# Optimization experiments

Measured on AMD Instinct MI355X. Metric: run time of the kernel, lower is better.

Reference implementation:

```python
import jax, jax.numpy as jnp
import numpy as np

N, E, P, D = 100000, 800000, 100000, 128

def setup_inputs() -> dict:
    key = jax.random.key(0)
    ks = jax.random.split(key, 24)
    def w(k, i, o):
        return jax.random.normal(k, (i, o), jnp.float32) * (1.0 / np.sqrt(i))
    inp = {
        'x': jax.random.normal(ks[0], (N, D), jnp.float32),
        'src': jax.random.randint(ks[1], (E,), 0, N, jnp.int32),
        'dst': jax.random.randint(ks[2], (E,), 0, N, jnp.int32),
        'pos_src': jax.random.randint(ks[3], (P,), 0, N, jnp.int32),
        'pos_dst': jax.random.randint(ks[4], (P,), 0, N, jnp.int32),
        'neg_src': jax.random.randint(ks[5], (P,), 0, N, jnp.int32),
        'neg_dst': jax.random.randint(ks[6], (P,), 0, N, jnp.int32),
        # SAGEConv params: fc_self, fc_neigh (+bias) per layer
        'Ws0': w(ks[7], D, D), 'Wn0': w(ks[8], D, D), 'b0': jnp.zeros((D,), jnp.float32),
        'Ws1': w(ks[9], D, D), 'Wn1': w(ks[10], D, D), 'b1': jnp.zeros((D,), jnp.float32),
        'Ws2': w(ks[11], D, D), 'Wn2': w(ks[12], D, D), 'b2': jnp.zeros((D,), jnp.float32),
        # predictor MLP: D->D->D->2
        'Wp0': w(ks[13], D, D), 'bp0': jnp.zeros((D,), jnp.float32),
        'Wp1': w(ks[14], D, D), 'bp1': jnp.zeros((D,), jnp.float32),
        'Wp2': w(ks[15], D, 2), 'bp2': jnp.zeros((2,), jnp.float32),
    }
    return inp

def _sage_layer(h, src, dst, n, Ws, Wn, b, act):
    # mean aggregation over in-neighbors (gather -> segment_sum -> divide)
    msum = jax.ops.segment_sum(h[src], dst, num_segments=n)      # [N, D]
    deg = jax.ops.segment_sum(jnp.ones_like(dst, jnp.float32), dst, num_segments=n)
    h_neigh = msum / jnp.maximum(deg, 1.0)[:, None]
    out = h @ Ws + h_neigh @ Wn + b
    return jax.nn.relu(out) if act else out

def _predict(hs, hd, Wp0, bp0, Wp1, bp1, Wp2, bp2):
    z = hs * hd
    z = jax.nn.relu(z @ Wp0 + bp0)
    z = jax.nn.relu(z @ Wp1 + bp1)
    return jax.nn.softmax(z @ Wp2 + bp2, axis=1)[:, 1]

def reference(x, src, dst, pos_src, pos_dst, neg_src, neg_dst,
              Ws0, Wn0, b0, Ws1, Wn1, b1, Ws2, Wn2, b2,
              Wp0, bp0, Wp1, bp1, Wp2, bp2):
    n = x.shape[0]
    h = _sage_layer(x, src, dst, n, Ws0, Wn0, b0, True)
    h = _sage_layer(h, src, dst, n, Ws1, Wn1, b1, True)
    h = _sage_layer(h, src, dst, n, Ws2, Wn2, b2, False)
    pos = _predict(h[pos_src], h[pos_dst], Wp0, bp0, Wp1, bp1, Wp2, bp2)
    neg = _predict(h[neg_src], h[neg_dst], Wp0, bp0, Wp1, bp1, Wp2, bp2)
    return (pos, neg)
```

## Files before the change

kernel.cpp:

```cpp
#include <hip/hip_runtime.h>
#include <cstdint>
#include <cstddef>
#include <cmath>

#define D 128

typedef short bf16x8 __attribute__((ext_vector_type(8)));
typedef float f32x4 __attribute__((ext_vector_type(4)));

__device__ __forceinline__ ushort f2b(float f) {
  uint x = __float_as_uint(f);
  uint r = ((x >> 16) & 1u) + 0x7fffu;
  return (ushort)((x + r) >> 16);
}
__device__ __forceinline__ float b2f(ushort u) {
  return __uint_as_float(((uint)u) << 16);
}

__device__ __forceinline__ void gl2lds16(const void* g, void* l) {
  __builtin_amdgcn_global_load_lds(
      (__attribute__((address_space(1))) void*)const_cast<void*>(g),
      (__attribute__((address_space(3))) void*)l, 16, 0, 0);
}

#define DB 1024
__global__ __launch_bounds__(256) void k_degree_conv(
    const int* __restrict__ dst, int E, int* __restrict__ deg,
    const float* __restrict__ in, ushort* __restrict__ outx, int n8, int cb,
    const float* __restrict__ Ws0, const float* __restrict__ Wn0,
    const float* __restrict__ Ws1, const float* __restrict__ Wn1,
    const float* __restrict__ Ws2, const float* __restrict__ Wn2,
    const float* __restrict__ Wp0, const float* __restrict__ Wp1,
    ushort* __restrict__ BpL0, ushort* __restrict__ BpL1, ushort* __restrict__ BpL2,
    ushort* __restrict__ BpP0, ushort* __restrict__ BpP1) {
  int b = blockIdx.x;
  if (b < DB) {
    for (int e = b * 256 + (int)threadIdx.x; e < E; e += DB * 256)
      atomicAdd(&deg[dst[e]], 1);
    return;
  }
  int b2 = b - DB;
  if (b2 < cb) {
    int i = b2 * 256 + threadIdx.x;
    if (i >= n8) return;
    float4 a = ((const float4*)in)[i * 2];
    float4 c = ((const float4*)in)[i * 2 + 1];
    ushort4 o0 = {f2b(a.x), f2b(a.y), f2b(a.z), f2b(a.w)};
    ushort4 o1 = {f2b(c.x), f2b(c.y), f2b(c.z), f2b(c.w)};
    ((ushort4*)outx)[i * 2] = o0;
    ((ushort4*)outx)[i * 2 + 1] = o1;
    return;
  }
  int o = (b2 - cb) * 256 + threadIdx.x;
  const float *W0, *W1; ushort* outp; int rel;
  if (o < 32768)       { W0 = Ws0; W1 = Wn0; outp = BpL0; rel = o; }
  else if (o < 65536)  { W0 = Ws1; W1 = Wn1; outp = BpL1; rel = o - 32768; }
  else if (o < 98304)  { W0 = Ws2; W1 = Wn2; outp = BpL2; rel = o - 65536; }
  else if (o < 114688) { W0 = Wp0; W1 = Wp0; outp = BpP0; rel = o - 98304; }
  else                 { W0 = Wp1; W1 = Wp1; outp = BpP1; rel = o - 114688; }
  int j = rel & 7, lane = (rel >> 3) & 63, t = (rel >> 9) & 7, ks = rel >> 12;
  int k = ks * 32 + ((lane >> 4) * 8) + j;
  int n = t * 16 + (lane & 15);
  const float* W = (k < 128) ? W0 : W1;
  int kk = (k < 128) ? k : k - 128;
  outp[rel] = f2b(W[(size_t)kk * D + n]);
}

__global__ __launch_bounds__(256) void k_fill_p(const int* __restrict__ src,
    const int* __restrict__ dst, int E, int* __restrict__ cursor,
    int* __restrict__ csrc, float scale, int CE) {
  int part = blockIdx.x & 7, chunk = blockIdx.x >> 3;
  long base = (long)chunk * CE;
  for (int i = threadIdx.x; i < CE; i += 256) {
    long e = base + i;
    if (e < E) {
      int d = dst[e];
      int p = (int)((float)d * scale); if (p > 7) p = 7;
      if (p == part) {
        int s = src[e];
        int pos = atomicAdd(&cursor[d], 1);
        csrc[pos] = s;
      }
    }
  }
}

#define SCAN_T 256
#define SCAN_E 4
#define SCAN_CHUNK (SCAN_T * SCAN_E)

__global__ void k_scan_partial(const int* __restrict__ deg, int n, int* __restrict__ part) {
  __shared__ int s[SCAN_T];
  int base = blockIdx.x * SCAN_CHUNK;
  int sum = 0;
  for (int i = 0; i < SCAN_E; ++i) {
    int idx = base + (int)threadIdx.x * SCAN_E + i;
    if (idx < n) sum += deg[idx];
  }
  s[threadIdx.x] = sum; __syncthreads();
  for (int ofs = SCAN_T / 2; ofs > 0; ofs >>= 1) {
    if ((int)threadIdx.x < ofs) s[threadIdx.x] += s[threadIdx.x + ofs];
    __syncthreads();
  }
  if (threadIdx.x == 0) part[blockIdx.x] = s[0];
}

__global__ void k_scan_final(const int* __restrict__ deg, int n, const int* __restrict__ part,
                             int nb, int* __restrict__ rowptr, int* __restrict__ cursor, int E) {
  __shared__ int s[SCAN_T];
  __shared__ int pbase;
  {
    int v = 0;
    for (int t = (int)threadIdx.x; t < (int)blockIdx.x; t += SCAN_T) v += part[t];
    s[threadIdx.x] = v; __syncthreads();
    for (int ofs = SCAN_T / 2; ofs > 0; ofs >>= 1) {
      if ((int)threadIdx.x < ofs) s[threadIdx.x] += s[threadIdx.x + ofs];
      __syncthreads();
    }
    if (threadIdx.x == 0) pbase = s[0];
    __syncthreads();
  }
  int base = blockIdx.x * SCAN_CHUNK;
  int v[SCAN_E]; int local = 0;
  for (int i = 0; i < SCAN_E; ++i) {
    int idx = base + (int)threadIdx.x * SCAN_E + i;
    v[i] = (idx < n) ? deg[idx] : 0;
    local += v[i];
  }
  s[threadIdx.x] = local; __syncthreads();
  for (int ofs = 1; ofs < SCAN_T; ofs <<= 1) {
    int t = ((int)threadIdx.x >= ofs) ? s[threadIdx.x - ofs] : 0;
    __syncthreads();
    s[threadIdx.x] += t;
    __syncthreads();
  }
  int run = pbase + s[threadIdx.x] - local;
  for (int i = 0; i < SCAN_E; ++i) {
    int idx = base + (int)threadIdx.x * SCAN_E + i;
    if (idx < n) { rowptr[idx] = run; cursor[idx] = run; }
    run += v[i];
  }
  if (blockIdx.x == 0 && threadIdx.x == 0) rowptr[n] = E;
}

#define SMS 136
__global__ __launch_bounds__(128, 4) void k_sage_fused(
    const ushort* __restrict__ A, const int* __restrict__ rowptr,
    const int* __restrict__ csrc, const ushort* __restrict__ Bp,
    const float* __restrict__ bias, ushort* __restrict__ out, int N, int do_relu) {
  __shared__ __align__(16) ushort smean[2][16][SMS];
  int tid = threadIdx.x, wave = tid >> 6, lane = tid & 63;
  int m = lane & 15, kg = lane >> 4;
  int g = kg, sub = m;
  int gb = g << 4;
  int row0 = (blockIdx.x * 2 + wave) * 16;
  uint hbo = (uint)(sub * 16);

  int node0 = row0 + g * 4;
  int rpv = 0;
  if (sub < 5) { int ix = node0 + sub; if (ix > N) ix = N; rpv = rowptr[ix]; }
  int beg[4], dgf[4], dd[4];
  #pragma unroll
  for (int j = 0; j < 4; ++j) {
    beg[j] = __shfl(rpv, gb + j);
    int endj = __shfl(rpv, gb + j + 1);
    dgf[j] = endj - beg[j];
    dd[j] = dgf[j] < 16 ? dgf[j] : 16;
  }
  int idxv[4];
  #pragma unroll
  for (int j = 0; j < 4; ++j) {
    int i = beg[j] + sub;
    idxv[j] = (sub < dgf[j]) ? csrc[i] : 0;
  }

  float f[4][8];
  #pragma unroll
  for (int j = 0; j < 4; ++j)
    #pragma unroll
    for (int q = 0; q < 8; ++q) f[j][q] = 0.f;

  int maxdd = dd[0];
  if (dd[1] > maxdd) maxdd = dd[1];
  if (dd[2] > maxdd) maxdd = dd[2];
  if (dd[3] > maxdd) maxdd = dd[3];

  uint off[4][4];
  #pragma unroll
  for (int j = 0; j < 4; ++j)
    #pragma unroll
    for (int k = 0; k < 4; ++k)
      off[j][k] = hbo + ((uint)__shfl(idxv[j], gb + k) << 8);

  #pragma unroll 1
  for (int e = 0; e < maxdd; e += 4) {
    bf16x8 r[4][4];
    #pragma unroll
    for (int j = 0; j < 4; ++j)
      #pragma unroll
      for (int k = 0; k < 4; ++k)
        r[j][k] = *(const bf16x8*)((const char*)A + off[j][k]);
    __builtin_amdgcn_sched_barrier(0);
    #pragma unroll
    for (int j = 0; j < 4; ++j)
      #pragma unroll
      for (int k = 0; k < 4; ++k) {
        int sl = e + 4 + k; sl = (sl > 15) ? 15 : sl;
        off[j][k] = hbo + ((uint)__shfl(idxv[j], gb + sl) << 8);
      }
    __builtin_amdgcn_sched_barrier(0);
    #pragma unroll
    for (int j = 0; j < 4; ++j) {
      #pragma unroll
      for (int k = 0; k < 4; ++k) {
        float w = (e + k < dd[j]) ? 1.0f : 0.0f;
        #pragma unroll
        for (int q = 0; q < 8; ++q) f[j][q] += w * b2f((ushort)r[j][k][q]);
      }
    }
  }
  #pragma unroll
  for (int j = 0; j < 4; ++j) {
    int endj = beg[j] + dgf[j];
    for (int i = beg[j] + 16; i < endj; ++i) {
      int s = csrc[i];
      bf16x8 v = *(const bf16x8*)((const char*)A + (hbo + ((uint)s << 8)));
      #pragma unroll
      for (int q = 0; q < 8; ++q) f[j][q] += b2f((ushort)v[q]);
    }
  }
  #pragma unroll
  for (int j = 0; j < 4; ++j) {
    float inv = (dgf[j] > 0) ? (1.0f / (float)dgf[j]) : 0.0f;
    bf16x8 o;
    #pragma unroll
    for (int q = 0; q < 8; ++q) o[q] = (short)f2b(f[j][q] * inv);
    *(bf16x8*)&smean[wave][g * 4 + j][sub * 8] = o;
  }
  asm volatile("s_waitcnt lgkmcnt(0)" ::: "memory");
  __builtin_amdgcn_sched_barrier(0);

  int ar = row0 + m; if (ar >= N) ar = N - 1;
  const ushort* a_self = A + (size_t)ar * D + kg * 8;
  f32x4 acc[8];
  #pragma unroll
  for (int t = 0; t < 8; ++t) acc[t] = f32x4{0.f, 0.f, 0.f, 0.f};
  #pragma unroll
  for (int ks = 0; ks < 8; ++ks) {
    bf16x8 af = (ks < 4) ? *(const bf16x8*)(a_self + ks * 32)
                         : *(const bf16x8*)&smean[wave][m][(ks - 4) * 32 + kg * 8];
    const ushort* bb = Bp + (size_t)ks * 4096 + lane * 8;
    #pragma unroll
    for (int t = 0; t < 8; ++t)
      acc[t] = __builtin_amdgcn_mfma_f32_16x16x32_bf16(af, *(const bf16x8*)(bb + t * 512), acc[t], 0, 0, 0);
  }
  #pragma unroll
  for (int t = 0; t < 8; ++t) {
    int c = t * 16 + m;
    float bv = bias[c];
    #pragma unroll
    for (int i = 0; i < 4; ++i) {
      int r = row0 + kg * 4 + i;
      float v = acc[t][i] + bv;
      if (do_relu) v = fmaxf(v, 0.f);
      if (r < N) out[(size_t)r * D + c] = f2b(v);
    }
  }
}

__global__ __launch_bounds__(256, 5) void k_predict_mfma(
    const ushort* __restrict__ h,
    const int* __restrict__ ps, const int* __restrict__ pd,
    const int* __restrict__ ns, const int* __restrict__ nd,
    const ushort* __restrict__ Bp0, const float* __restrict__ bp0,
    const ushort* __restrict__ Bp1, const float* __restrict__ bp1,
    const float* __restrict__ Wp2, const float* __restrict__ bp2,
    float* __restrict__ outp, int P, int pb) {
  __shared__ __align__(1024) ushort slab[4][4096];
  int bi = blockIdx.x;
  const int* sidx; const int* didx; float* op;
  if (bi >= pb) { sidx = ns; didx = nd; op = outp + P; bi -= pb; }
  else          { sidx = ps; didx = pd; op = outp; }
  int tid = threadIdx.x;
  int wave = tid >> 6, lane = tid & 63;
  int m = lane & 15, kg = lane >> 4;
  int pair0 = bi * 64 + wave * 16;
  int prow = pair0 + m; int pr = (prow < P) ? prow : P - 1;
  int si = sidx[pr], di = didx[pr];
  char* sl = (char*)&slab[wave][0];

  {
    int rsub = lane >> 4;
    #pragma unroll
    for (int q = 0; q < 4; ++q) {
      int rr = q * 4 + rsub;
      int ir = __shfl(si, rr);
      const char* g = (const char*)h + ((size_t)(uint)ir << 8)
                      + (uint)((((lane & 15) ^ (rr & 7)) << 4));
      gl2lds16(g, sl + (q << 10));
    }
    #pragma unroll
    for (int q = 0; q < 4; ++q) {
      int rr = q * 4 + rsub;
      int ir = __shfl(di, rr);
      const char* g = (const char*)h + ((size_t)(uint)ir << 8)
                      + (uint)((((lane & 15) ^ (rr & 7)) << 4));
      gl2lds16(g, sl + 4096 + (q << 10));
    }
  }
  __syncthreads();

  f32x4 acc[8];
  #pragma unroll
  for (int t = 0; t < 8; ++t) acc[t] = f32x4{0.f, 0.f, 0.f, 0.f};
  #pragma unroll
  for (int ks = 0; ks < 4; ++ks) {
    int slot = (ks * 4 + kg) ^ (m & 7);
    const char* rbase = sl + m * 256 + slot * 16;
    bf16x8 as8 = *(const bf16x8*)rbase;
    bf16x8 ad8 = *(const bf16x8*)(rbase + 4096);
    bf16x8 af;
    #pragma unroll
    for (int j = 0; j < 8; ++j) {
      float p = b2f((ushort)as8[j]) * b2f((ushort)ad8[j]);
      af[j] = (short)f2b(p);
    }
    const ushort* bb = Bp0 + (size_t)ks * 4096 + lane * 8;
    #pragma unroll
    for (int t = 0; t < 8; ++t)
      acc[t] = __builtin_amdgcn_mfma_f32_16x16x32_bf16(af, *(const bf16x8*)(bb + t * 512), acc[t], 0, 0, 0);
  }
  ushort* zp = (ushort*)sl;
  #pragma unroll
  for (int t = 0; t < 8; ++t) {
    int c = t * 16 + m;
    float bv = bp0[c];
    int ks2 = c >> 5, kg2 = (c >> 3) & 3, j2 = c & 7;
    #pragma unroll
    for (int i = 0; i < 4; ++i) {
      float v = fmaxf(acc[t][i] + bv, 0.f);
      int l2 = kg2 * 16 + kg * 4 + i;
      zp[(ks2 * 64 + l2) * 8 + j2] = f2b(v);
    }
  }
  asm volatile("s_waitcnt lgkmcnt(0)" ::: "memory");
  __builtin_amdgcn_sched_barrier(0);
  #pragma unroll
  for (int t = 0; t < 8; ++t) acc[t] = f32x4{0.f, 0.f, 0.f, 0.f};
  #pragma unroll
  for (int ks = 0; ks < 4; ++ks) {
    bf16x8 af = *(const bf16x8*)(zp + (ks * 64 + lane) * 8);
    const ushort* bb = Bp1 + (size_t)ks * 4096 + lane * 8;
    #pragma unroll
    for (int t = 0; t < 8; ++t)
      acc[t] = __builtin_amdgcn_mfma_f32_16x16x32_bf16(af, *(const bf16x8*)(bb + t * 512), acc[t], 0, 0, 0);
  }
  float p0[4] = {0.f, 0.f, 0.f, 0.f}, p1[4] = {0.f, 0.f, 0.f, 0.f};
  #pragma unroll
  for (int t = 0; t < 8; ++t) {
    int c = t * 16 + m;
    float bv = bp1[c];
    float wa = Wp2[(size_t)c * 2], wb = Wp2[(size_t)c * 2 + 1];
    #pragma unroll
    for (int i = 0; i < 4; ++i) {
      float z = fmaxf(acc[t][i] + bv, 0.f);
      p0[i] += z * wa;
      p1[i] += z * wb;
    }
  }
  #pragma unroll
  for (int msk = 1; msk <= 8; msk <<= 1) {
    #pragma unroll
    for (int i = 0; i < 4; ++i) {
      p0[i] += __shfl_xor(p0[i], msk);
      p1[i] += __shfl_xor(p1[i], msk);
    }
  }
  if (m == 0) {
    float c0 = bp2[0], c1 = bp2[1];
    #pragma unroll
    for (int i = 0; i < 4; ++i) {
      int r = pair0 + kg * 4 + i;
      if (r < P) {
        float l0 = p0[i] + c0, l1 = p1[i] + c1;
        op[r] = 1.0f / (1.0f + expf(l0 - l1));
      }
    }
  }
}

extern "C" void kernel_launch(void* const* d_in, const int* in_sizes, int n_in,
                              void* d_out, int out_size, void* d_ws, size_t ws_size,
                              hipStream_t stream) {
  const float* x       = (const float*)d_in[0];
  const int*   src     = (const int*)d_in[1];
  const int*   dst     = (const int*)d_in[2];
  const int*   pos_src = (const int*)d_in[3];
  const int*   pos_dst = (const int*)d_in[4];
  const int*   neg_src = (const int*)d_in[5];
  const int*   neg_dst = (const int*)d_in[6];
  const float* Ws0 = (const float*)d_in[7],  *Wn0 = (const float*)d_in[8],  *b0 = (const float*)d_in[9];
  const float* Ws1 = (const float*)d_in[10], *Wn1 = (const float*)d_in[11], *b1 = (const float*)d_in[12];
  const float* Ws2 = (const float*)d_in[13], *Wn2 = (const float*)d_in[14], *b2 = (const float*)d_in[15];
  const float* Wp0 = (const float*)d_in[16], *bp0 = (const float*)d_in[17];
  const float* Wp1 = (const float*)d_in[18], *bp1 = (const float*)d_in[19];
  const float* Wp2 = (const float*)d_in[20], *bp2 = (const float*)d_in[21];
  const int N = in_sizes[0] / D;
  const int E = in_sizes[1];
  const int P = in_sizes[3];
  float* outp = (float*)d_out;

  char* ws = (char*)d_ws;
  size_t off = 0;
  auto alloc = [&](size_t bytes) -> void* {
    void* p = ws + off;
    off += (bytes + 255) & ~(size_t)255;
    return p;
  };
  ushort* xb    = (ushort*)alloc((size_t)N * D * 2);
  ushort* h1    = (ushort*)alloc((size_t)N * D * 2);
  ushort* h2    = (ushort*)alloc((size_t)N * D * 2);
  ushort* BpL0  = (ushort*)alloc(256 * D * 2);
  ushort* BpL1  = (ushort*)alloc(256 * D * 2);
  ushort* BpL2  = (ushort*)alloc(256 * D * 2);
  ushort* BpP0  = (ushort*)alloc(128 * D * 2);
  ushort* BpP1  = (ushort*)alloc(128 * D * 2);
  int*    deg    = (int*)alloc((size_t)N * 4);
  int*    rowptr = (int*)alloc((size_t)(N + 1) * 4);
  int*    cursor = (int*)alloc((size_t)N * 4);
  int*    part   = (int*)alloc(4096);
  int*    csrc   = (int*)alloc((size_t)E * 4);
  (void)ws_size; (void)n_in; (void)out_size;

  const float pscale = 8.0f / (float)N;
  const int CB = 96;
  const int CE = (E + CB - 1) / CB;

  hipMemsetAsync(deg, 0, (size_t)N * 4, stream);
  int n8 = N * D / 8;
  int cb = (n8 + 255) / 256;
  k_degree_conv<<<DB + cb + 512, 256, 0, stream>>>(
      dst, E, deg,
      x, xb, n8, cb,
      Ws0, Wn0, Ws1, Wn1, Ws2, Wn2, Wp0, Wp1,
      BpL0, BpL1, BpL2, BpP0, BpP1);

  int nb = (N + SCAN_CHUNK - 1) / SCAN_CHUNK;
  k_scan_partial<<<nb, SCAN_T, 0, stream>>>(deg, N, part);
  k_scan_final<<<nb, SCAN_T, 0, stream>>>(deg, N, part, nb, rowptr, cursor, E);
  k_fill_p<<<8 * CB, 256, 0, stream>>>(src, dst, E, cursor, csrc, pscale, CE);

  int gemb = (N + 31) / 32;
  k_sage_fused<<<gemb, 128, 0, stream>>>(xb, rowptr, csrc, BpL0, b0, h1, N, 1);
  k_sage_fused<<<gemb, 128, 0, stream>>>(h1, rowptr, csrc, BpL1, b1, h2, N, 1);
  k_sage_fused<<<gemb, 128, 0, stream>>>(h2, rowptr, csrc, BpL2, b2, xb, N, 0);

  int pb = (P + 63) / 64;
  k_predict_mfma<<<2 * pb, 256, 0, stream>>>(xb, pos_src, pos_dst, neg_src, neg_dst,
                                             BpP0, bp0, BpP1, bp1, Wp2, bp2, outp, P, pb);
}
```

Measured before the change: 445.4 us.

## Replace CSR build with fixed-slot per-node adjacency and overflow spill list

Drops the degree-count, two-pass scan and separate fill kernels. Edges are instead written straight into 32 fixed slots per destination node, with a global spill list for any overflow, all inside the fused conversion kernel. This removes three launches and one full pass over the edge list. The cost is a padded adjacency array of N*32 ints with sparser gather reads, and a linear scan of the spill list for high-degree nodes. Edges are silently dropped if the spill list exceeds its cap.

```diff
diff --git a/kernel.cpp b/kernel.cpp
--- a/kernel.cpp
+++ b/kernel.cpp
@@ -4,6 +4,8 @@
 #include <cmath>
 
 #define D 128
+#define SLOTS 32
+#define SPILL_CAP 65536
 
 typedef short bf16x8 __attribute__((ext_vector_type(8)));
 typedef float f32x4 __attribute__((ext_vector_type(4)));
@@ -23,9 +25,11 @@
       (__attribute__((address_space(3))) void*)l, 16, 0, 0);
 }
 
-#define DB 1024
-__global__ __launch_bounds__(256) void k_degree_conv(
-    const int* __restrict__ dst, int E, int* __restrict__ deg,
+__global__ __launch_bounds__(256) void k_fill_conv(
+    const int* __restrict__ src, const int* __restrict__ dst, int E,
+    int* __restrict__ cnt, int* __restrict__ csrc,
+    int* __restrict__ spillc, int* __restrict__ spill_d, int* __restrict__ spill_s,
+    float scale, int CE,
     const float* __restrict__ in, ushort* __restrict__ outx, int n8, int cb,
     const float* __restrict__ Ws0, const float* __restrict__ Wn0,
     const float* __restrict__ Ws1, const float* __restrict__ Wn1,
@@ -34,12 +38,29 @@
     ushort* __restrict__ BpL0, ushort* __restrict__ BpL1, ushort* __restrict__ BpL2,
     ushort* __restrict__ BpP0, ushort* __restrict__ BpP1) {
   int b = blockIdx.x;
-  if (b < DB) {
-    for (int e = b * 256 + (int)threadIdx.x; e < E; e += DB * 256)
-      atomicAdd(&deg[dst[e]], 1);
+  if (b < 768) {
+    int part = b & 7, chunk = b >> 3;
+    long base = (long)chunk * CE;
+    for (int i = threadIdx.x; i < CE; i += 256) {
+      long e = base + i;
+      if (e < E) {
+        int d = dst[e];
+        int p = (int)((float)d * scale); if (p > 7) p = 7;
+        if (p == part) {
+          int s = src[e];
+          int pos = atomicAdd(&cnt[d], 1);
+          if (pos < SLOTS) {
+            csrc[((size_t)d << 5) + pos] = s;
+          } else {
+            int si = atomicAdd(spillc, 1);
+            if (si < SPILL_CAP) { spill_d[si] = d; spill_s[si] = s; }
+          }
+        }
+      }
+    }
     return;
   }
-  int b2 = b - DB;
+  int b2 = b - 768;
   if (b2 < cb) {
     int i = b2 * 256 + threadIdx.x;
     if (i >= n8) return;
@@ -66,87 +87,12 @@
   outp[rel] = f2b(W[(size_t)kk * D + n]);
 }
 
-__global__ __launch_bounds__(256) void k_fill_p(const int* __restrict__ src,
-    const int* __restrict__ dst, int E, int* __restrict__ cursor,
-    int* __restrict__ csrc, float scale, int CE) {
-  int part = blockIdx.x & 7, chunk = blockIdx.x >> 3;
-  long base = (long)chunk * CE;
-  for (int i = threadIdx.x; i < CE; i += 256) {
-    long e = base + i;
-    if (e < E) {
-      int d = dst[e];
-      int p = (int)((float)d * scale); if (p > 7) p = 7;
-      if (p == part) {
-        int s = src[e];
-        int pos = atomicAdd(&cursor[d], 1);
-        csrc[pos] = s;
-      }
-    }
-  }
-}
-
-#define SCAN_T 256
-#define SCAN_E 4
-#define SCAN_CHUNK (SCAN_T * SCAN_E)
-
-__global__ void k_scan_partial(const int* __restrict__ deg, int n, int* __restrict__ part) {
-  __shared__ int s[SCAN_T];
-  int base = blockIdx.x * SCAN_CHUNK;
-  int sum = 0;
-  for (int i = 0; i < SCAN_E; ++i) {
-    int idx = base + (int)threadIdx.x * SCAN_E + i;
-    if (idx < n) sum += deg[idx];
-  }
-  s[threadIdx.x] = sum; __syncthreads();
-  for (int ofs = SCAN_T / 2; ofs > 0; ofs >>= 1) {
-    if ((int)threadIdx.x < ofs) s[threadIdx.x] += s[threadIdx.x + ofs];
-    __syncthreads();
-  }
-  if (threadIdx.x == 0) part[blockIdx.x] = s[0];
-}
-
-__global__ void k_scan_final(const int* __restrict__ deg, int n, const int* __restrict__ part,
-                             int nb, int* __restrict__ rowptr, int* __restrict__ cursor, int E) {
-  __shared__ int s[SCAN_T];
-  __shared__ int pbase;
-  {
-    int v = 0;
-    for (int t = (int)threadIdx.x; t < (int)blockIdx.x; t += SCAN_T) v += part[t];
-    s[threadIdx.x] = v; __syncthreads();
-    for (int ofs = SCAN_T / 2; ofs > 0; ofs >>= 1) {
-      if ((int)threadIdx.x < ofs) s[threadIdx.x] += s[threadIdx.x + ofs];
-      __syncthreads();
-    }
-    if (threadIdx.x == 0) pbase = s[0];
-    __syncthreads();
-  }
-  int base = blockIdx.x * SCAN_CHUNK;
-  int v[SCAN_E]; int local = 0;
-  for (int i = 0; i < SCAN_E; ++i) {
-    int idx = base + (int)threadIdx.x * SCAN_E + i;
-    v[i] = (idx < n) ? deg[idx] : 0;
-    local += v[i];
-  }
-  s[threadIdx.x] = local; __syncthreads();
-  for (int ofs = 1; ofs < SCAN_T; ofs <<= 1) {
-    int t = ((int)threadIdx.x >= ofs) ? s[threadIdx.x - ofs] : 0;
-    __syncthreads();
-    s[threadIdx.x] += t;
-    __syncthreads();
-  }
-  int run = pbase + s[threadIdx.x] - local;
-  for (int i = 0; i < SCAN_E; ++i) {
-    int idx = base + (int)threadIdx.x * SCAN_E + i;
-    if (idx < n) { rowptr[idx] = run; cursor[idx] = run; }
-    run += v[i];
-  }
-  if (blockIdx.x == 0 && threadIdx.x == 0) rowptr[n] = E;
-}
-
 #define SMS 136
 __global__ __launch_bounds__(128, 4) void k_sage_fused(
-    const ushort* __restrict__ A, const int* __restrict__ rowptr,
-    const int* __restrict__ csrc, const ushort* __restrict__ Bp,
+    const ushort* __restrict__ A, const int* __restrict__ cnt,
+    const int* __restrict__ csrc,
+    const int* __restrict__ spillc, const int* __restrict__ spill_d,
+    const int* __restrict__ spill_s, const ushort* __restrict__ Bp,
     const float* __restrict__ bias, ushort* __restrict__ out, int N, int do_relu) {
   __shared__ __align__(16) ushort smean[2][16][SMS];
   int tid = threadIdx.x, wave = tid >> 6, lane = tid & 63;
@@ -157,21 +103,18 @@
   uint hbo = (uint)(sub * 16);
 
   int node0 = row0 + g * 4;
-  int rpv = 0;
-  if (sub < 5) { int ix = node0 + sub; if (ix > N) ix = N; rpv = rowptr[ix]; }
-  int beg[4], dgf[4], dd[4];
+  int cv = 0;
+  if (sub < 4) { int ix = node0 + sub; if (ix < N) cv = cnt[ix]; }
+  int dgf[4], dd[4];
   #pragma unroll
   for (int j = 0; j < 4; ++j) {
-    beg[j] = __shfl(rpv, gb + j);
-    int endj = __shfl(rpv, gb + j + 1);
-    dgf[j] = endj - beg[j];
+    dgf[j] = __shfl(cv, gb + j);
     dd[j] = dgf[j] < 16 ? dgf[j] : 16;
   }
   int idxv[4];
   #pragma unroll
   for (int j = 0; j < 4; ++j) {
-    int i = beg[j] + sub;
-    idxv[j] = (sub < dgf[j]) ? csrc[i] : 0;
+    idxv[j] = (sub < dgf[j]) ? csrc[((size_t)(uint)(node0 + j) << 5) + sub] : 0;
   }
 
   float f[4][8];
@@ -221,12 +164,24 @@
   }
   #pragma unroll
   for (int j = 0; j < 4; ++j) {
-    int endj = beg[j] + dgf[j];
-    for (int i = beg[j] + 16; i < endj; ++i) {
-      int s = csrc[i];
+    int nd = node0 + j;
+    int lim = dgf[j] < SLOTS ? dgf[j] : SLOTS;
+    for (int i = 16; i < lim; ++i) {
+      int s = csrc[((size_t)(uint)nd << 5) + i];
       bf16x8 v = *(const bf16x8*)((const char*)A + (hbo + ((uint)s << 8)));
       #pragma unroll
       for (int q = 0; q < 8; ++q) f[j][q] += b2f((ushort)v[q]);
+    }
+    if (dgf[j] > SLOTS) {
+      int sc = *spillc; if (sc > SPILL_CAP) sc = SPILL_CAP;
+      for (int i = 0; i < sc; ++i) {
+        if (spill_d[i] == nd) {
+          int s = spill_s[i];
+          bf16x8 v = *(const bf16x8*)((const char*)A + (hbo + ((uint)s << 8)));
+          #pragma unroll
+          for (int q = 0; q < 8; ++q) f[j][q] += b2f((ushort)v[q]);
+        }
+      }
     }
   }
   #pragma unroll
@@ -425,35 +380,33 @@
   ushort* BpL2  = (ushort*)alloc(256 * D * 2);
   ushort* BpP0  = (ushort*)alloc(128 * D * 2);
   ushort* BpP1  = (ushort*)alloc(128 * D * 2);
-  int*    deg    = (int*)alloc((size_t)N * 4);
-  int*    rowptr = (int*)alloc((size_t)(N + 1) * 4);
-  int*    cursor = (int*)alloc((size_t)N * 4);
-  int*    part   = (int*)alloc(4096);
-  int*    csrc   = (int*)alloc((size_t)E * 4);
+  int*    cnt     = (int*)alloc((size_t)(N + 64) * 4);
+  int*    csrc    = (int*)alloc((size_t)N * SLOTS * 4);
+  int*    spill_d = (int*)alloc((size_t)SPILL_CAP * 4);
+  int*    spill_s = (int*)alloc((size_t)SPILL_CAP * 4);
+  int*    spillc  = cnt + N;
   (void)ws_size; (void)n_in; (void)out_size;
 
   const float pscale = 8.0f / (float)N;
   const int CB = 96;
   const int CE = (E + CB - 1) / CB;
 
-  hipMemsetAsync(deg, 0, (size_t)N * 4, stream);
+  hipMemsetAsync(cnt, 0, (size_t)(N + 64) * 4, stream);
   int n8 = N * D / 8;
   int cb = (n8 + 255) / 256;
-  k_degree_conv<<<DB + cb + 512, 256, 0, stream>>>(
-      dst, E, deg,
+  k_fill_conv<<<768 + cb + 512, 256, 0, stream>>>(
+      src, dst, E, cnt, csrc, spillc, spill_d, spill_s, pscale, CE,
       x, xb, n8, cb,
       Ws0, Wn0, Ws1, Wn1, Ws2, Wn2, Wp0, Wp1,
       BpL0, BpL1, BpL2, BpP0, BpP1);
 
-  int nb = (N + SCAN_CHUNK - 1) / SCAN_CHUNK;
-  k_scan_partial<<<nb, SCAN_T, 0, stream>>>(deg, N, part);
-  k_scan_final<<<nb, SCAN_T, 0, stream>>>(deg, N, part, nb, rowptr, cursor, E);
-  k_fill_p<<<8 * CB, 256, 0, stream>>>(src, dst, E, cursor, csrc, pscale, CE);
-
   int gemb = (N + 31) / 32;
-  k_sage_fused<<<gemb, 128, 0, stream>>>(xb, rowptr, csrc, BpL0, b0, h1, N, 1);
-  k_sage_fused<<<gemb, 128, 0, stream>>>(h1, rowptr, csrc, BpL1, b1, h2, N, 1);
-  k_sage_fused<<<gemb, 128, 0, stream>>>(h2, rowptr, csrc, BpL2, b2, xb, N, 0);
+  k_sage_fused<<<gemb, 128, 0, stream>>>(xb, cnt, csrc, spillc, spill_d, spill_s,
+                                         BpL0, b0, h1, N, 1);
+  k_sage_fused<<<gemb, 128, 0, stream>>>(h1, cnt, csrc, spillc, spill_d, spill_s,
+                                         BpL1, b1, h2, N, 1);
+  k_sage_fused<<<gemb, 128, 0, stream>>>(h2, cnt, csrc, spillc, spill_d, spill_s,
+                                         BpL2, b2, xb, N, 0);
 
   int pb = (P + 63) / 64;
   k_predict_mfma<<<2 * pb, 256, 0, stream>>>(xb, pos_src, pos_dst, neg_src, neg_dst,
```

Result: slower. 566.4 us (+27.2%).
